# Kernel optimization log

Hardware: AMD Instinct MI355X
Metric: run time of the kernel (lower is better)

Reference implementation:

```python
import jax, jax.numpy as jnp
import numpy as np

# Model dims (match init_kwargs / Mamba2 defaults)
D_MODEL = 1024
D_STATE = 128
D_CONV = 4
EXPAND = 2
HEADDIM = 64
NGROUPS = 1
D_INNER = EXPAND * D_MODEL            # 2048
NHEADS = D_INNER // HEADDIM           # 32
D_IN_PROJ = 2 * D_INNER + 2 * NGROUPS * D_STATE + NHEADS  # 4384 (d_mlp == 0)
CONV_DIM = D_INNER + 2 * NGROUPS * D_STATE                 # 2304
BATCH = 2
SEQLEN = 512
EPS = 1e-5


def _silu(x):
    return x * jax.nn.sigmoid(x)


def setup_inputs() -> dict:
    key = jax.random.key(0)
    ks = jax.random.split(key, 8)
    u = jax.random.normal(ks[0], (BATCH, SEQLEN, D_MODEL), jnp.float32)
    W_in = jax.random.normal(ks[1], (D_IN_PROJ, D_MODEL), jnp.float32) * (D_MODEL ** -0.5)
    conv_w = jax.random.normal(ks[2], (CONV_DIM, 1, D_CONV), jnp.float32) * (D_CONV ** -0.5)
    conv_b = jnp.zeros((CONV_DIM,), jnp.float32)
    # dt_bias init as in the torch module (inverse-softplus of dt in [dt_min, dt_max])
    dt = jnp.exp(jax.random.uniform(ks[3], (NHEADS,), jnp.float32)
                 * (np.log(0.1) - np.log(0.001)) + np.log(0.001))
    dt = jnp.clip(dt, 1e-4, None)
    dt_bias = dt + jnp.log(-jnp.expm1(-dt))
    A_log = jnp.log(jax.random.uniform(ks[4], (NHEADS,), jnp.float32, minval=1.0, maxval=16.0))
    D_param = jnp.ones((NHEADS,), jnp.float32)
    norm_w = jnp.ones((D_INNER,), jnp.float32)
    W_out = jax.random.normal(ks[5], (D_MODEL, D_INNER), jnp.float32) * (D_INNER ** -0.5)
    return dict(u=u, W_in=W_in, conv_w=conv_w, conv_b=conv_b, dt_bias=dt_bias,
                A_log=A_log, D_param=D_param, norm_w=norm_w, W_out=W_out)


def reference(u, W_in, conv_w, conv_b, dt_bias, A_log, D_param, norm_w, W_out):
    B, L, _ = u.shape
    # in_proj (no bias): [B,L,d_in_proj]
    zxbcdt = jnp.einsum('bld,ed->ble', u, W_in)
    z = zxbcdt[..., :D_INNER]
    xBC = zxbcdt[..., D_INNER:D_INNER + CONV_DIM]
    dt = zxbcdt[..., D_INNER + CONV_DIM:]          # [B,L,H]

    # causal depthwise conv1d (pad left d_conv-1 == conv padding + slice in torch)
    xc = jnp.transpose(xBC, (0, 2, 1))             # [B,C,L]
    xc = jax.lax.conv_general_dilated(
        xc, conv_w, window_strides=(1,), padding=[(D_CONV - 1, 0)],
        dimension_numbers=('NCH', 'OIH', 'NCH'), feature_group_count=CONV_DIM)
    xc = xc + conv_b[None, :, None]
    xBC = _silu(jnp.transpose(xc, (0, 2, 1)))      # [B,L,C]

    x = xBC[..., :D_INNER].reshape(B, L, NHEADS, HEADDIM)
    Bv = xBC[..., D_INNER:D_INNER + NGROUPS * D_STATE].reshape(B, L, NGROUPS, D_STATE)
    Cv = xBC[..., D_INNER + NGROUPS * D_STATE:].reshape(B, L, NGROUPS, D_STATE)

    A = -jnp.exp(A_log)                            # [H]
    dt = jax.nn.softplus(dt + dt_bias)             # [B,L,H]

    def step(state, inp):
        dt_t, x_t, B_t, C_t = inp                  # [B,H],[B,H,P],[B,G,N],[B,G,N]
        dA = jnp.exp(dt_t * A)                     # [B,H]
        dBx = jnp.einsum('bh,bgn,bhp->bhpn', dt_t, B_t, x_t)
        state = state * dA[:, :, None, None] + dBx
        y = jnp.einsum('bhpn,bgn->bhp', state, C_t) + D_param[:, None] * x_t
        return state, y

    state0 = jnp.zeros((B, NHEADS, HEADDIM, D_STATE), u.dtype)
    xs = (jnp.moveaxis(dt, 1, 0), jnp.moveaxis(x, 1, 0),
          jnp.moveaxis(Bv, 1, 0), jnp.moveaxis(Cv, 1, 0))
    _, ys = jax.lax.scan(step, state0, xs)         # ys: [L,B,H,P]
    y = jnp.moveaxis(ys, 0, 1).reshape(B, L, D_INNER)

    # RMSNormGated, norm_before_gate=False: gate first, then rmsnorm
    yg = y * _silu(z)
    yn = yg * jax.lax.rsqrt(jnp.mean(yg * yg, axis=-1, keepdims=True) + EPS) * norm_w

    return jnp.einsum('bld,ed->ble', yn, W_out)    # out_proj, no bias
```

## Files before the change

### kernel.cpp

```cpp
#include <hip/hip_runtime.h>
#include <hip/hip_bf16.h>

#define D_MODEL   1024
#define D_STATE   128
#define D_INNER   2048
#define NHEADS    32
#define HEADDIM   64
#define D_IN_PROJ 4384
#define NPROJ_PAD 4480
#define CONV_DIM  2304
#define BATCH     2
#define SEQLEN    512
#define M_TOKENS  (BATCH*SEQLEN)
#define EPS       1e-5f
#define LC        64
#define NCH       (SEQLEN/LC)

typedef __bf16 bf16x8 __attribute__((ext_vector_type(8)));
typedef float  f32x4  __attribute__((ext_vector_type(4)));

__device__ __forceinline__ ushort f2bf(float f) {
  union { float f; unsigned int i; } v; v.f = f;
  unsigned int x = v.i;
  return (ushort)((x + 0x7fffu + ((x >> 16) & 1u)) >> 16);
}
__device__ __forceinline__ float bf2f(ushort u) {
  union { unsigned int i; float f; } v; v.i = ((unsigned int)u) << 16; return v.f;
}

__device__ __forceinline__ void gload_lds16u(const ushort* g, ushort* l) {
  __builtin_amdgcn_global_load_lds(
      (const __attribute__((address_space(1))) void*)g,
      (__attribute__((address_space(3))) void*)l, 16, 0, 0);
}

__device__ __forceinline__ void cvt8(const float* __restrict__ s,
                                     ushort* __restrict__ d, int i) {
  const float4 a = *(const float4*)(s + i);
  const float4 b = *(const float4*)(s + i + 4);
  uint4 v;
  v.x = (unsigned)f2bf(a.x) | ((unsigned)f2bf(a.y) << 16);
  v.y = (unsigned)f2bf(a.z) | ((unsigned)f2bf(a.w) << 16);
  v.z = (unsigned)f2bf(b.x) | ((unsigned)f2bf(b.y) << 16);
  v.w = (unsigned)f2bf(b.z) | ((unsigned)f2bf(b.w) << 16);
  *(uint4*)(d + i) = v;
}
__global__ __launch_bounds__(256) void cvt3(const float* __restrict__ s0, ushort* __restrict__ d0, int n0,
                                            const float* __restrict__ s1, ushort* __restrict__ d1, int n1,
                                            const float* __restrict__ s2, ushort* __restrict__ d2, int n2) {
  const int i = (blockIdx.x * 256 + threadIdx.x) * 8;
  if (i < n0)                cvt8(s0, d0, i);
  else if (i < n0 + n1)      cvt8(s1, d1, i - n0);
  else if (i < n0 + n1 + n2) cvt8(s2, d2, i - n0 - n1);
}

template <int BM, int BN, int MASK_N>
__global__ __launch_bounds__(256) void gemm_tile(const ushort* __restrict__ A,
                                                 const ushort* __restrict__ Bt,
                                                 float* __restrict__ C,
                                                 int Nreal, int K, int ldc) {
  constexpr int WM = BM / 2, WN = BN / 2, FM = WM / 16, FN = WN / 16;
  constexpr int LA = BM * 4 / 256, LB = BN * 4 / 256;
  __shared__ ushort As[BM * 32];
  __shared__ ushort Bs[BN * 32];
  const int tid = threadIdx.x, lane = tid & 63, wave = tid >> 6;
  const int r16 = lane & 15, q = lane >> 4;
  const int wm = wave & 1, wn = wave >> 1;
  const int m0 = blockIdx.y * BM, n0 = blockIdx.x * BN;

  f32x4 acc[FM][FN] = {};

  for (int k0 = 0; k0 < K; k0 += 32) {
    __syncthreads();
    #pragma unroll
    for (int it = 0; it < LA; ++it) {
      const int idx = it * 256 + tid;
      gload_lds16u(A + (size_t)(m0 + (idx >> 2)) * K + k0 + (idx & 3) * 8,
                   As + (it * 256 + wave * 64) * 8);
    }
    #pragma unroll
    for (int it = 0; it < LB; ++it) {
      const int idx = it * 256 + tid;
      gload_lds16u(Bt + (size_t)(n0 + (idx >> 2)) * K + k0 + (idx & 3) * 8,
                   Bs + (it * 256 + wave * 64) * 8);
    }
    __syncthreads();

    bf16x8 af[FM], bfr[FN];
    #pragma unroll
    for (int i = 0; i < FM; ++i)
      af[i] = *(const bf16x8*)(const void*)(As + (wm * WM + i * 16 + r16) * 32 + q * 8);
    #pragma unroll
    for (int j = 0; j < FN; ++j)
      bfr[j] = *(const bf16x8*)(const void*)(Bs + (wn * WN + j * 16 + r16) * 32 + q * 8);
    #pragma unroll
    for (int i = 0; i < FM; ++i)
      #pragma unroll
      for (int j = 0; j < FN; ++j)
        acc[i][j] = __builtin_amdgcn_mfma_f32_16x16x32_bf16(af[i], bfr[j], acc[i][j], 0, 0, 0);
  }

  #pragma unroll
  for (int i = 0; i < FM; ++i) {
    const int row = m0 + wm * WM + i * 16 + q * 4;
    #pragma unroll
    for (int j = 0; j < FN; ++j) {
      const int col = n0 + wn * WN + j * 16 + r16;
      if (!MASK_N || col < Nreal) {
        #pragma unroll
        for (int r = 0; r < 4; ++r)
          C[(size_t)(row + r) * ldc + col] = acc[i][j][r];
      }
    }
  }
}

__global__ __launch_bounds__(256) void gemm_sk(const ushort* __restrict__ A,
                                               const ushort* __restrict__ Bt,
                                               float* __restrict__ C,
                                               int Khalf, int ldab, int ldc) {
  __shared__ ushort As[64 * 32];
  __shared__ ushort Bs[64 * 32];
  const int tid = threadIdx.x, lane = tid & 63, wave = tid >> 6;
  const int r16 = lane & 15, q = lane >> 4;
  const int wm = wave & 1, wn = wave >> 1;
  const int m0 = blockIdx.y * 64, n0 = blockIdx.x * 64;
  const int kb = blockIdx.z * Khalf;

  f32x4 acc[2][2] = {};
  for (int k0 = 0; k0 < Khalf; k0 += 32) {
    __syncthreads();
    gload_lds16u(A + (size_t)(m0 + (tid >> 2)) * ldab + kb + k0 + (tid & 3) * 8,
                 As + (tid & ~63) * 8 );
    gload_lds16u(Bt + (size_t)(n0 + (tid >> 2)) * ldab + kb + k0 + (tid & 3) * 8,
                 Bs + (tid & ~63) * 8);
    __syncthreads();

    bf16x8 af[2], bfr[2];
    #pragma unroll
    for (int i = 0; i < 2; ++i)
      af[i] = *(const bf16x8*)(const void*)(As + (wm * 32 + i * 16 + r16) * 32 + q * 8);
    #pragma unroll
    for (int j = 0; j < 2; ++j)
      bfr[j] = *(const bf16x8*)(const void*)(Bs + (wn * 32 + j * 16 + r16) * 32 + q * 8);
    #pragma unroll
    for (int i = 0; i < 2; ++i)
      #pragma unroll
      for (int j = 0; j < 2; ++j)
        acc[i][j] = __builtin_amdgcn_mfma_f32_16x16x32_bf16(af[i], bfr[j], acc[i][j], 0, 0, 0);
  }

  #pragma unroll
  for (int i = 0; i < 2; ++i) {
    const int row = m0 + wm * 32 + i * 16 + q * 4;
    #pragma unroll
    for (int j = 0; j < 2; ++j) {
      const int col = n0 + wn * 32 + j * 16 + r16;
      #pragma unroll
      for (int r = 0; r < 4; ++r)
        unsafeAtomicAdd(&C[(size_t)(row + r) * ldc + col], acc[i][j][r]);
    }
  }
}

__global__ __launch_bounds__(256) void conv_silu(const float* __restrict__ zx,
                                                 const float* __restrict__ cw,
                                                 const float* __restrict__ cb,
                                                 float* __restrict__ xbc,
                                                 ushort* __restrict__ BCbf) {
  const int idx = blockIdx.x * 256 + threadIdx.x;
  const int c   = idx % CONV_DIM;
  const int bt  = idx / CONV_DIM;
  const int t   = bt % SEQLEN;

  float acc = cb[c];
  #pragma unroll
  for (int k = 0; k < 4; ++k) {
    const int tt = t - 3 + k;
    if (tt >= 0) {
      acc += zx[(size_t)(bt - 3 + k) * D_IN_PROJ + D_INNER + c] * cw[c * 4 + k];
    }
  }
  const float s = acc / (1.f + __expf(-acc));
  xbc[idx] = s;
  if (c >= D_INNER) BCbf[(size_t)bt * 256 + (c - D_INNER)] = f2bf(s);
}

__global__ __launch_bounds__(512) void dtcsum(const float* __restrict__ zx,
                                              const float* __restrict__ dt_bias,
                                              const float* __restrict__ A_log,
                                              float* __restrict__ dts,
                                              float* __restrict__ csum) {
  const int bh = blockIdx.x;
  const int b = bh >> 5, h = bh & 31;
  const int t = threadIdx.x;
  const float raw = zx[(size_t)(b * SEQLEN + t) * D_IN_PROJ + (D_INNER + CONV_DIM) + h]
                  + dt_bias[h];
  const float sp = (raw > 20.f) ? raw : log1pf(__expf(raw));
  const float An = -__expf(A_log[h]);
  float x = sp * An;
  #pragma unroll
  for (int off = 1; off < 64; off <<= 1) {
    const float v = __shfl_up(x, off);
    if ((t & 63) >= off) x += v;
  }
  dts[(size_t)bh * SEQLEN + t]  = sp;
  csum[(size_t)bh * SEQLEN + t] = x;
}

__global__ __launch_bounds__(256) void chunk_intra(const float* __restrict__ xbc,
                                                   const ushort* __restrict__ BCbf,
                                                   const float* __restrict__ dts,
                                                   const float* __restrict__ csum,
                                                   ushort* __restrict__ Yi,
                                                   ushort* __restrict__ dS) {
  const int blk = blockIdx.x;
  const int c = blk & 7, h = (blk >> 3) & 31, b = blk >> 8;
  const int bh = b * 32 + h;
  const int tid = threadIdx.x, lane = tid & 63, wave = tid >> 6;
  const int r16 = lane & 15, q = lane >> 4;

  __shared__ ushort Ml[64 * 72];
  __shared__ ushort Xt[64 * 72];
  __shared__ ushort Bw[128 * 72];
  __shared__ float dtl[LC], csl[LC];

  if (tid < LC) {
    dtl[tid] = dts[(size_t)bh * SEQLEN + c * LC + tid];
    csl[tid] = csum[(size_t)bh * SEQLEN + c * LC + tid];
  }
  __syncthreads();
  const float cs63 = csl[LC - 1];

  const ushort* Cp = BCbf + (size_t)(b * SEQLEN + c * LC + wave * 16 + r16) * 256 + 128 + q * 8;
  const ushort* Bp = BCbf + (size_t)(b * SEQLEN + c * LC + r16) * 256 + q * 8;
  f32x4 g[4] = {};
  #pragma unroll
  for (int kk = 0; kk < 4; ++kk) {
    const bf16x8 a = *(const bf16x8*)(const void*)(Cp + kk * 32);
    #pragma unroll
    for (int j = 0; j < 4; ++j) {
      const bf16x8 bb = *(const bf16x8*)(const void*)(Bp + (size_t)j * 16 * 256 + kk * 32);
      g[j] = __builtin_amdgcn_mfma_f32_16x16x32_bf16(a, bb, g[j], 0, 0, 0);
    }
  }
  float cst[4];
  #pragma unroll
  for (int r = 0; r < 4; ++r) cst[r] = csl[wave * 16 + q * 4 + r];
  #pragma unroll
  for (int j = 0; j < 4; ++j) {
    const int s = j * 16 + r16;
    const float ds_ = dtl[s], css = csl[s];
    #pragma unroll
    for (int r = 0; r < 4; ++r) {
      const int t = wave * 16 + q * 4 + r;
      const float v = (s <= t) ? g[j][r] * ds_ * __expf(cst[r] - css) : 0.f;
      Ml[t * 72 + s] = f2bf(v);
    }
  }

  const float* xb = xbc + (size_t)(b * SEQLEN + c * LC) * CONV_DIM + h * HEADDIM;
  #pragma unroll
  for (int i = 0; i < 16; ++i) {
    const int idx = i * 256 + tid;
    const int s = idx >> 6, p = idx & 63;
    Xt[p * 72 + s] = f2bf(xb[(size_t)s * CONV_DIM + p]);
  }
  const float* Bb = xbc + (size_t)(b * SEQLEN + c * LC) * CONV_DIM + D_INNER;
  #pragma unroll
  for (int i = 0; i < 32; ++i) {
    const int idx = i * 256 + tid;
    const int s = idx >> 7, n = idx & 127;
    const float w = dtl[s] * __expf(cs63 - csl[s]);
    Bw[n * 72 + s] = f2bf(Bb[(size_t)s * CONV_DIM + n] * w);
  }
  __syncthreads();

  f32x4 accY[4] = {};
  f32x4 accS[2][4] = {};
  #pragma unroll
  for (int kk = 0; kk < 2; ++kk) {
    const bf16x8 am = *(const bf16x8*)(const void*)(Ml + (wave * 16 + r16) * 72 + kk * 32 + q * 8);
    const bf16x8 a0 = *(const bf16x8*)(const void*)(Bw + (wave * 32 + r16) * 72 + kk * 32 + q * 8);
    const bf16x8 a1 = *(const bf16x8*)(const void*)(Bw + (wave * 32 + 16 + r16) * 72 + kk * 32 + q * 8);
    #pragma unroll
    for (int j = 0; j < 4; ++j) {
      const bf16x8 bx = *(const bf16x8*)(const void*)(Xt + (j * 16 + r16) * 72 + kk * 32 + q * 8);
      accY[j]    = __builtin_amdgcn_mfma_f32_16x16x32_bf16(am, bx, accY[j], 0, 0, 0);
      accS[0][j] = __builtin_amdgcn_mfma_f32_16x16x32_bf16(a0, bx, accS[0][j], 0, 0, 0);
      accS[1][j] = __builtin_amdgcn_mfma_f32_16x16x32_bf16(a1, bx, accS[1][j], 0, 0, 0);
    }
  }

  ushort* Yp = Yi + (size_t)blk * 4096;
  #pragma unroll
  for (int j = 0; j < 4; ++j)
    #pragma unroll
    for (int r = 0; r < 4; ++r)
      Yp[(wave * 16 + q * 4 + r) * 64 + j * 16 + r16] = f2bf(accY[j][r]);

  ushort* Sp = dS + (size_t)blk * 8192;
  #pragma unroll
  for (int u = 0; u < 2; ++u)
    #pragma unroll
    for (int j = 0; j < 4; ++j)
      #pragma unroll
      for (int r = 0; r < 4; ++r)
        Sp[(wave * 32 + u * 16 + q * 4 + r) * 64 + j * 16 + r16] = f2bf(accS[u][j][r]);
}

__global__ __launch_bounds__(256) void chunk_state(const ushort* __restrict__ dS,
                                                   const float* __restrict__ csum,
                                                   ushort* __restrict__ St) {
  const int bh = blockIdx.x;
  const int tid = threadIdx.x;
  const int p = tid & 63, n0 = (tid >> 6) * 32;
  float S[32] = {};
  for (int c = 0; c < NCH; ++c) {
    const size_t base = ((size_t)bh * 8 + c) * 8192;
    uint4 pk[4];
    unsigned* pw = (unsigned*)pk;
    #pragma unroll
    for (int j = 0; j < 16; ++j)
      pw[j] = (unsigned)f2bf(S[2 * j]) | ((unsigned)f2bf(S[2 * j + 1]) << 16);
    uint4* dst = (uint4*)(St + base + (size_t)p * 128 + n0);
    #pragma unroll
    for (int j = 0; j < 4; ++j) dst[j] = pk[j];
    const float e = __expf(csum[(size_t)bh * SEQLEN + c * LC + (LC - 1)]);
    #pragma unroll
    for (int j = 0; j < 32; ++j) {
      const float d = bf2f(dS[base + (size_t)(n0 + j) * 64 + p]);
      S[j] = S[j] * e + d;
    }
  }
}

__global__ __launch_bounds__(256) void chunk_inter(const ushort* __restrict__ BCbf,
                                                   const ushort* __restrict__ St,
                                                   const ushort* __restrict__ Yi,
                                                   const float* __restrict__ xbc,
                                                   const float* __restrict__ csum,
                                                   const float* __restrict__ Dp,
                                                   float* __restrict__ y) {
  const int blk = blockIdx.x;
  const int c = blk & 7, h = (blk >> 3) & 31, b = blk >> 8;
  const int bh = b * 32 + h;
  const int tid = threadIdx.x, lane = tid & 63, wave = tid >> 6;
  const int r16 = lane & 15, q = lane >> 4;

  const ushort* Cp = BCbf + (size_t)(b * SEQLEN + c * LC + wave * 16 + r16) * 256 + 128 + q * 8;
  const ushort* Sp = St + (size_t)blk * 8192 + (size_t)r16 * 128 + q * 8;
  f32x4 acc[4] = {};
  #pragma unroll
  for (int kk = 0; kk < 4; ++kk) {
    const bf16x8 a = *(const bf16x8*)(const void*)(Cp + kk * 32);
    #pragma unroll
    for (int j = 0; j < 4; ++j) {
      const bf16x8 bb = *(const bf16x8*)(const void*)(Sp + (size_t)j * 16 * 128 + kk * 32);
      acc[j] = __builtin_amdgcn_mfma_f32_16x16x32_bf16(a, bb, acc[j], 0, 0, 0);
    }
  }

  const float Dh = Dp[h];
  const ushort* Yp = Yi + (size_t)blk * 4096;
  float sc[4];
  #pragma unroll
  for (int r = 0; r < 4; ++r)
    sc[r] = __expf(csum[(size_t)bh * SEQLEN + c * LC + wave * 16 + q * 4 + r]);
  #pragma unroll
  for (int j = 0; j < 4; ++j) {
    const int col = j * 16 + r16;
    #pragma unroll
    for (int r = 0; r < 4; ++r) {
      const int t = wave * 16 + q * 4 + r;
      const size_t row = (size_t)(b * SEQLEN + c * LC + t);
      const float xv = xbc[row * CONV_DIM + h * HEADDIM + col];
      y[row * D_INNER + h * HEADDIM + col] =
          acc[j][r] * sc[r] + bf2f(Yp[t * 64 + col]) + Dh * xv;
    }
  }
}

__global__ __launch_bounds__(256) void gate_norm(const float* __restrict__ y,
                                                 const float* __restrict__ zx,
                                                 const float* __restrict__ nw,
                                                 ushort* __restrict__ yn) {
  const int row = blockIdx.x;
  const int tid = threadIdx.x;
  float vals[8];
  float ss = 0.f;
  #pragma unroll
  for (int i = 0; i < 8; ++i) {
    const int e = tid + i * 256;
    const float yv = y[(size_t)row * D_INNER + e];
    const float z = zx[(size_t)row * D_IN_PROJ + e];
    const float g = z / (1.f + __expf(-z));
    const float yg = yv * g;
    vals[i] = yg;
    ss = fmaf(yg, yg, ss);
  }
  for (int o = 32; o > 0; o >>= 1) ss += __shfl_down(ss, o);
  __shared__ float wsum[4];
  if ((tid & 63) == 0) wsum[tid >> 6] = ss;
  __syncthreads();
  const float tot = wsum[0] + wsum[1] + wsum[2] + wsum[3];
  const float rms = rsqrtf(tot * (1.f / D_INNER) + EPS);
  #pragma unroll
  for (int i = 0; i < 8; ++i) {
    const int e = tid + i * 256;
    yn[(size_t)row * D_INNER + e] = f2bf(vals[i] * rms * nw[e]);
  }
}

extern "C" void kernel_launch(void* const* d_in, const int* in_sizes, int n_in,
                              void* d_out, int out_size, void* d_ws, size_t ws_size,
                              hipStream_t stream) {
  const float* u       = (const float*)d_in[0];
  const float* W_in    = (const float*)d_in[1];
  const float* conv_w  = (const float*)d_in[2];
  const float* conv_b  = (const float*)d_in[3];
  const float* dt_bias = (const float*)d_in[4];
  const float* A_log   = (const float*)d_in[5];
  const float* D_par   = (const float*)d_in[6];
  const float* norm_w  = (const float*)d_in[7];
  const float* W_out   = (const float*)d_in[8];
  float* out = (float*)d_out;

  char* ws = (char*)d_ws;
  float*  zx      = (float*)ws;
  float*  xbc     = (float*)(ws + 17956864);
  float*  yb      = (float*)(ws + 27394048);
  ushort* yn      = (ushort*)(ws + 35782656);
  ushort* u_bf    = (ushort*)(ws + 39976960);
  ushort* Win_bf  = (ushort*)(ws + 42074112);
  ushort* Yi      = (ushort*)(ws + 39976960);
  ushort* Wout_bf = (ushort*)(ws + 51052544);
  ushort* BC_bf   = (ushort*)(ws + 55246848);
  float*  dts     = (float*)(ws + 55771136);
  float*  csum    = (float*)(ws + 55902208);
  ushort* dS      = (ushort*)(ws + 56295424);
  ushort* St      = (ushort*)(ws + 64684032);

  hipMemsetAsync(out, 0, (size_t)M_TOKENS * D_MODEL * sizeof(float), stream);

  const int n_u = M_TOKENS * D_MODEL, n_wi = D_IN_PROJ * D_MODEL, n_wo = D_MODEL * D_INNER;
  cvt3<<<(n_u + n_wi + n_wo) / (256 * 8), 256, 0, stream>>>(
      u, u_bf, n_u, W_in, Win_bf, n_wi, W_out, Wout_bf, n_wo);

  gemm_tile<128, 64, 1><<<dim3(NPROJ_PAD / 64, M_TOKENS / 128), 256, 0, stream>>>(
      u_bf, Win_bf, zx, D_IN_PROJ, D_MODEL, D_IN_PROJ);
  conv_silu<<<(M_TOKENS * CONV_DIM) / 256, 256, 0, stream>>>(zx, conv_w, conv_b, xbc, BC_bf);

  dtcsum<<<BATCH * NHEADS, 512, 0, stream>>>(zx, dt_bias, A_log, dts, csum);
  chunk_intra<<<BATCH * NHEADS * NCH, 256, 0, stream>>>(xbc, BC_bf, dts, csum, Yi, dS);
  chunk_state<<<BATCH * NHEADS, 256, 0, stream>>>(dS, csum, St);
  chunk_inter<<<BATCH * NHEADS * NCH, 256, 0, stream>>>(BC_bf, St, Yi, xbc, csum, D_par, yb);

  gate_norm<<<M_TOKENS, 256, 0, stream>>>(yb, zx, norm_w, yn);
  gemm_sk<<<dim3(D_MODEL / 64, M_TOKENS / 64, 2), 256, 0, stream>>>(
      yn, Wout_bf, out, D_INNER / 2, D_INNER, D_MODEL);
}
```

Before: 194.4 us.

## Fuse gate and RMSNorm into chunk_inter epilogue and out-proj GEMM; merge conv and dt kernels

Removes the separate gate_norm kernel. chunk_inter now applies the SiLU(z) gate, writes the gated y directly as bf16, and atomically accumulates per-row sums of squares. The out-proj GEMM scales by rsqrt of those sums in its epilogue, and norm_w is folded into the bf16 W_out during conversion. Conv+SiLU and the dt softplus/cumsum are merged into one launch, with a sliding window over time so each thread reuses loaded values. In exchange this adds an extra memset and atomics, and rounds the un-normalized gated y to bf16 before scaling.

```diff
diff --git a/kernel.cpp b/kernel.cpp
--- a/kernel.cpp
+++ b/kernel.cpp
@@ -47,11 +47,25 @@
 }
 __global__ __launch_bounds__(256) void cvt3(const float* __restrict__ s0, ushort* __restrict__ d0, int n0,
                                             const float* __restrict__ s1, ushort* __restrict__ d1, int n1,
-                                            const float* __restrict__ s2, ushort* __restrict__ d2, int n2) {
+                                            const float* __restrict__ s2, ushort* __restrict__ d2, int n2,
+                                            const float* __restrict__ nw) {
   const int i = (blockIdx.x * 256 + threadIdx.x) * 8;
-  if (i < n0)                cvt8(s0, d0, i);
-  else if (i < n0 + n1)      cvt8(s1, d1, i - n0);
-  else if (i < n0 + n1 + n2) cvt8(s2, d2, i - n0 - n1);
+  if (i < n0)           cvt8(s0, d0, i);
+  else if (i < n0 + n1) cvt8(s1, d1, i - n0);
+  else if (i < n0 + n1 + n2) {
+    const int j = i - n0 - n1;
+    const int k = j & (D_INNER - 1);
+    const float4 a = *(const float4*)(s2 + j);
+    const float4 b = *(const float4*)(s2 + j + 4);
+    const float4 wa = *(const float4*)(nw + k);
+    const float4 wb = *(const float4*)(nw + k + 4);
+    uint4 v;
+    v.x = (unsigned)f2bf(a.x * wa.x) | ((unsigned)f2bf(a.y * wa.y) << 16);
+    v.y = (unsigned)f2bf(a.z * wa.z) | ((unsigned)f2bf(a.w * wa.w) << 16);
+    v.z = (unsigned)f2bf(b.x * wb.x) | ((unsigned)f2bf(b.y * wb.y) << 16);
+    v.w = (unsigned)f2bf(b.z * wb.z) | ((unsigned)f2bf(b.w * wb.w) << 16);
+    *(uint4*)(d2 + j) = v;
+  }
 }
 
 template <int BM, int BN, int MASK_N>
@@ -118,6 +132,7 @@
 __global__ __launch_bounds__(256) void gemm_sk(const ushort* __restrict__ A,
                                                const ushort* __restrict__ Bt,
                                                float* __restrict__ C,
+                                               const float* __restrict__ sumsq,
                                                int Khalf, int ldab, int ldc) {
   __shared__ ushort As[64 * 32];
   __shared__ ushort Bs[64 * 32];
@@ -131,7 +146,7 @@
   for (int k0 = 0; k0 < Khalf; k0 += 32) {
     __syncthreads();
     gload_lds16u(A + (size_t)(m0 + (tid >> 2)) * ldab + kb + k0 + (tid & 3) * 8,
-                 As + (tid & ~63) * 8 );
+                 As + (tid & ~63) * 8);
     gload_lds16u(Bt + (size_t)(n0 + (tid >> 2)) * ldab + kb + k0 + (tid & 3) * 8,
                  Bs + (tid & ~63) * 8);
     __syncthreads();
@@ -153,59 +168,76 @@
   #pragma unroll
   for (int i = 0; i < 2; ++i) {
     const int row = m0 + wm * 32 + i * 16 + q * 4;
+    float rms[4];
+    #pragma unroll
+    for (int r = 0; r < 4; ++r)
+      rms[r] = rsqrtf(sumsq[row + r] * (1.f / D_INNER) + EPS);
     #pragma unroll
     for (int j = 0; j < 2; ++j) {
       const int col = n0 + wn * 32 + j * 16 + r16;
       #pragma unroll
       for (int r = 0; r < 4; ++r)
-        unsafeAtomicAdd(&C[(size_t)(row + r) * ldc + col], acc[i][j][r]);
-    }
-  }
-}
-
-__global__ __launch_bounds__(256) void conv_silu(const float* __restrict__ zx,
-                                                 const float* __restrict__ cw,
-                                                 const float* __restrict__ cb,
-                                                 float* __restrict__ xbc,
-                                                 ushort* __restrict__ BCbf) {
-  const int idx = blockIdx.x * 256 + threadIdx.x;
-  const int c   = idx % CONV_DIM;
-  const int bt  = idx / CONV_DIM;
-  const int t   = bt % SEQLEN;
-
-  float acc = cb[c];
-  #pragma unroll
-  for (int k = 0; k < 4; ++k) {
-    const int tt = t - 3 + k;
-    if (tt >= 0) {
-      acc += zx[(size_t)(bt - 3 + k) * D_IN_PROJ + D_INNER + c] * cw[c * 4 + k];
-    }
-  }
-  const float s = acc / (1.f + __expf(-acc));
-  xbc[idx] = s;
-  if (c >= D_INNER) BCbf[(size_t)bt * 256 + (c - D_INNER)] = f2bf(s);
-}
-
-__global__ __launch_bounds__(512) void dtcsum(const float* __restrict__ zx,
-                                              const float* __restrict__ dt_bias,
-                                              const float* __restrict__ A_log,
-                                              float* __restrict__ dts,
-                                              float* __restrict__ csum) {
-  const int bh = blockIdx.x;
-  const int b = bh >> 5, h = bh & 31;
-  const int t = threadIdx.x;
-  const float raw = zx[(size_t)(b * SEQLEN + t) * D_IN_PROJ + (D_INNER + CONV_DIM) + h]
-                  + dt_bias[h];
-  const float sp = (raw > 20.f) ? raw : log1pf(__expf(raw));
-  const float An = -__expf(A_log[h]);
-  float x = sp * An;
-  #pragma unroll
-  for (int off = 1; off < 64; off <<= 1) {
-    const float v = __shfl_up(x, off);
-    if ((t & 63) >= off) x += v;
-  }
-  dts[(size_t)bh * SEQLEN + t]  = sp;
-  csum[(size_t)bh * SEQLEN + t] = x;
+        unsafeAtomicAdd(&C[(size_t)(row + r) * ldc + col], acc[i][j][r] * rms[r]);
+    }
+  }
+}
+
+__global__ __launch_bounds__(256) void conv_dt(const float* __restrict__ zx,
+                                               const float* __restrict__ cw,
+                                               const float* __restrict__ cb,
+                                               float* __restrict__ xbc,
+                                               ushort* __restrict__ BCbf,
+                                               const float* __restrict__ dt_bias,
+                                               const float* __restrict__ A_log,
+                                               float* __restrict__ dts,
+                                               float* __restrict__ csum) {
+  const int blk = blockIdx.x;
+  if (blk < 1152) {
+    const int g  = blk / 9;
+    const int c  = (blk % 9) * 256 + threadIdx.x;
+    const int b  = g >> 6;
+    const int t0 = (g & 63) * 8;
+    const float4 w4 = *(const float4*)(cw + c * 4);
+    const float bias = cb[c];
+    const float* col = zx + (size_t)(b * SEQLEN) * D_IN_PROJ + D_INNER + c;
+    float win[11];
+    #pragma unroll
+    for (int k = 0; k < 11; ++k) {
+      const int t = t0 - 3 + k;
+      win[k] = (t >= 0) ? col[(size_t)t * D_IN_PROJ] : 0.f;
+    }
+    #pragma unroll
+    for (int i = 0; i < 8; ++i) {
+      float a = bias;
+      a = fmaf(win[i],     w4.x, a);
+      a = fmaf(win[i + 1], w4.y, a);
+      a = fmaf(win[i + 2], w4.z, a);
+      a = fmaf(win[i + 3], w4.w, a);
+      const float s = a / (1.f + __expf(-a));
+      const size_t bt = (size_t)(b * SEQLEN + t0 + i);
+      xbc[bt * CONV_DIM + c] = s;
+      if (c >= D_INNER) BCbf[bt * 256 + (c - D_INNER)] = f2bf(s);
+    }
+  } else {
+    const int bh = blk - 1152;
+    const int b = bh >> 5, h = bh & 31;
+    const int wave = threadIdx.x >> 6, lane = threadIdx.x & 63;
+    const float dtb = dt_bias[h];
+    const float An  = -__expf(A_log[h]);
+    for (int cc = wave; cc < NCH; cc += 4) {
+      const int t = cc * LC + lane;
+      const float raw = zx[(size_t)(b * SEQLEN + t) * D_IN_PROJ + (D_INNER + CONV_DIM) + h] + dtb;
+      const float sp = (raw > 20.f) ? raw : log1pf(__expf(raw));
+      float x = sp * An;
+      #pragma unroll
+      for (int off = 1; off < 64; off <<= 1) {
+        const float v = __shfl_up(x, off);
+        if (lane >= off) x += v;
+      }
+      dts[(size_t)bh * SEQLEN + t]  = sp;
+      csum[(size_t)bh * SEQLEN + t] = x;
+    }
+  }
 }
 
 __global__ __launch_bounds__(256) void chunk_intra(const float* __restrict__ xbc,
@@ -339,9 +371,11 @@
                                                    const ushort* __restrict__ St,
                                                    const ushort* __restrict__ Yi,
                                                    const float* __restrict__ xbc,
+                                                   const float* __restrict__ zx,
                                                    const float* __restrict__ csum,
                                                    const float* __restrict__ Dp,
-                                                   float* __restrict__ y) {
+                                                   ushort* __restrict__ yn,
+                                                   float* __restrict__ sumsq) {
   const int blk = blockIdx.x;
   const int c = blk & 7, h = (blk >> 3) & 31, b = blk >> 8;
   const int bh = b * 32 + h;
@@ -363,7 +397,7 @@
 
   const float Dh = Dp[h];
   const ushort* Yp = Yi + (size_t)blk * 4096;
-  float sc[4];
+  float sc[4], ssq[4] = {0.f, 0.f, 0.f, 0.f};
   #pragma unroll
   for (int r = 0; r < 4; ++r)
     sc[r] = __expf(csum[(size_t)bh * SEQLEN + c * LC + wave * 16 + q * 4 + r]);
@@ -375,40 +409,24 @@
       const int t = wave * 16 + q * 4 + r;
       const size_t row = (size_t)(b * SEQLEN + c * LC + t);
       const float xv = xbc[row * CONV_DIM + h * HEADDIM + col];
-      y[row * D_INNER + h * HEADDIM + col] =
-          acc[j][r] * sc[r] + bf2f(Yp[t * 64 + col]) + Dh * xv;
-    }
-  }
-}
-
-__global__ __launch_bounds__(256) void gate_norm(const float* __restrict__ y,
-                                                 const float* __restrict__ zx,
-                                                 const float* __restrict__ nw,
-                                                 ushort* __restrict__ yn) {
-  const int row = blockIdx.x;
-  const int tid = threadIdx.x;
-  float vals[8];
-  float ss = 0.f;
-  #pragma unroll
-  for (int i = 0; i < 8; ++i) {
-    const int e = tid + i * 256;
-    const float yv = y[(size_t)row * D_INNER + e];
-    const float z = zx[(size_t)row * D_IN_PROJ + e];
-    const float g = z / (1.f + __expf(-z));
-    const float yg = yv * g;
-    vals[i] = yg;
-    ss = fmaf(yg, yg, ss);
-  }
-  for (int o = 32; o > 0; o >>= 1) ss += __shfl_down(ss, o);
-  __shared__ float wsum[4];
-  if ((tid & 63) == 0) wsum[tid >> 6] = ss;
-  __syncthreads();
-  const float tot = wsum[0] + wsum[1] + wsum[2] + wsum[3];
-  const float rms = rsqrtf(tot * (1.f / D_INNER) + EPS);
-  #pragma unroll
-  for (int i = 0; i < 8; ++i) {
-    const int e = tid + i * 256;
-    yn[(size_t)row * D_INNER + e] = f2bf(vals[i] * rms * nw[e]);
+      const float yv = acc[j][r] * sc[r] + bf2f(Yp[t * 64 + col]) + Dh * xv;
+      const float z  = zx[row * D_IN_PROJ + h * HEADDIM + col];
+      const float yg = yv * (z / (1.f + __expf(-z)));
+      yn[row * D_INNER + h * HEADDIM + col] = f2bf(yg);
+      ssq[r] = fmaf(yg, yg, ssq[r]);
+    }
+  }
+  #pragma unroll
+  for (int o = 1; o < 16; o <<= 1) {
+    #pragma unroll
+    for (int r = 0; r < 4; ++r) ssq[r] += __shfl_xor(ssq[r], o);
+  }
+  if (r16 == 0) {
+    #pragma unroll
+    for (int r = 0; r < 4; ++r) {
+      const int t = wave * 16 + q * 4 + r;
+      unsafeAtomicAdd(&sumsq[b * SEQLEN + c * LC + t], ssq[r]);
+    }
   }
 }
 
@@ -429,7 +447,7 @@
   char* ws = (char*)d_ws;
   float*  zx      = (float*)ws;
   float*  xbc     = (float*)(ws + 17956864);
-  float*  yb      = (float*)(ws + 27394048);
+  float*  sumsq   = (float*)(ws + 27394048);
   ushort* yn      = (ushort*)(ws + 35782656);
   ushort* u_bf    = (ushort*)(ws + 39976960);
   ushort* Win_bf  = (ushort*)(ws + 42074112);
@@ -442,21 +460,22 @@
   ushort* St      = (ushort*)(ws + 64684032);
 
   hipMemsetAsync(out, 0, (size_t)M_TOKENS * D_MODEL * sizeof(float), stream);
+  hipMemsetAsync(sumsq, 0, (size_t)M_TOKENS * sizeof(float), stream);
 
   const int n_u = M_TOKENS * D_MODEL, n_wi = D_IN_PROJ * D_MODEL, n_wo = D_MODEL * D_INNER;
   cvt3<<<(n_u + n_wi + n_wo) / (256 * 8), 256, 0, stream>>>(
-      u, u_bf, n_u, W_in, Win_bf, n_wi, W_out, Wout_bf, n_wo);
+      u, u_bf, n_u, W_in, Win_bf, n_wi, W_out, Wout_bf, n_wo, norm_w);
 
   gemm_tile<128, 64, 1><<<dim3(NPROJ_PAD / 64, M_TOKENS / 128), 256, 0, stream>>>(
       u_bf, Win_bf, zx, D_IN_PROJ, D_MODEL, D_IN_PROJ);
-  conv_silu<<<(M_TOKENS * CONV_DIM) / 256, 256, 0, stream>>>(zx, conv_w, conv_b, xbc, BC_bf);
-
-  dtcsum<<<BATCH * NHEADS, 512, 0, stream>>>(zx, dt_bias, A_log, dts, csum);
+  conv_dt<<<1152 + 64, 256, 0, stream>>>(zx, conv_w, conv_b, xbc, BC_bf,
+                                         dt_bias, A_log, dts, csum);
+
   chunk_intra<<<BATCH * NHEADS * NCH, 256, 0, stream>>>(xbc, BC_bf, dts, csum, Yi, dS);
   chunk_state<<<BATCH * NHEADS, 256, 0, stream>>>(dS, csum, St);
-  chunk_inter<<<BATCH * NHEADS * NCH, 256, 0, stream>>>(BC_bf, St, Yi, xbc, csum, D_par, yb);
-
-  gate_norm<<<M_TOKENS, 256, 0, stream>>>(yb, zx, norm_w, yn);
+  chunk_inter<<<BATCH * NHEADS * NCH, 256, 0, stream>>>(BC_bf, St, Yi, xbc, zx,
+                                                        csum, D_par, yn, sumsq);
+
   gemm_sk<<<dim3(D_MODEL / 64, M_TOKENS / 64, 2), 256, 0, stream>>>(
-      yn, Wout_bf, out, D_INNER / 2, D_INNER, D_MODEL);
-}
+      yn, Wout_bf, out, sumsq, D_INNER / 2, D_INNER, D_MODEL);
+}
```

New measurement: 188.9 us. -2.8%, faster.
